# Kernel tuning notes

Hardware: AMD Instinct MI355X
Metric: run time of the kernel (lower is better)

The kernel has to match this reference:

```python
import jax, jax.numpy as jnp
import numpy as np

NUM_USERS = 100000
NUM_ITEMS = 50000
LATENT_DIM = 64
N_EDGES = 600000
BATCH = 4096
N_LAYERS = 4  # K=4, time_split=4, euler -> 4 unit propagation steps


def setup_inputs() -> dict:
    key = jax.random.key(0)
    k1, k2, k3, k4, k5, k6 = jax.random.split(key, 6)
    return {
        "users": jax.random.randint(k1, (BATCH,), 0, NUM_USERS),
        "items": jax.random.randint(k2, (BATCH,), 0, NUM_ITEMS),
        "edge_u": jax.random.randint(k3, (N_EDGES,), 0, NUM_USERS),
        "edge_i": jax.random.randint(k4, (N_EDGES,), 0, NUM_ITEMS),
        "user_emb": 0.1 * jax.random.normal(k5, (NUM_USERS, LATENT_DIM), dtype=jnp.float32),
        "item_emb": 0.1 * jax.random.normal(k6, (NUM_ITEMS, LATENT_DIM), dtype=jnp.float32),
    }


def reference(users, items, edge_u, edge_i, user_emb, item_emb):
    num_users = user_emb.shape[0]
    num_items = item_emb.shape[0]
    N = num_users + num_items

    # symmetric bipartite adjacency as directed edge list
    src = jnp.concatenate([edge_u, edge_i + num_users])
    dst = jnp.concatenate([edge_i + num_users, edge_u])

    # D^{-1/2} A D^{-1/2} edge weights (LightGCN normalization)
    deg = jax.ops.segment_sum(jnp.ones_like(src, dtype=jnp.float32), src, num_segments=N)
    inv_sqrt = jnp.where(deg > 0, jax.lax.rsqrt(jnp.maximum(deg, 1.0)), 0.0)
    w = inv_sqrt[src] * inv_sqrt[dst]  # [2E]

    def spmm(x):  # A_hat @ x via gather-scale-scatter
        return jax.ops.segment_sum(w[:, None] * x[src], dst, num_segments=N)

    x0 = jnp.concatenate([user_emb, item_emb], axis=0)  # [N, d]
    # ODE euler step x + A x, then residual subtraction -> stored emb = A^k x0
    embs = [x0]
    e = x0
    for _ in range(N_LAYERS):
        e = spmm(e)
        embs.append(e)
    light_out = jnp.mean(jnp.stack(embs, axis=1), axis=1)  # [N, d]

    all_users = light_out[:num_users]
    all_items = light_out[num_users:]
    users_emb = all_users[users]
    items_emb = all_items[items]
    gamma = jnp.sum(users_emb * items_emb, axis=1)  # [B]
    return gamma
```

## Files before the change

kernel.cpp:

```cpp
#include <hip/hip_runtime.h>

#define WAVE 64
#define BROWS 256
#define NBKT_MAX 1024
#define CMAX 4
#define SRCMASK 0x3FFFF
#define EPB 2048
#define ENTCAP 4096


__device__ __forceinline__ unsigned short f2bf(float f) {
    unsigned u = __float_as_uint(f);
    u += 0x7FFF + ((u >> 16) & 1);
    return (unsigned short)(u >> 16);
}
__device__ __forceinline__ float bf2f(unsigned short v) {
    return __uint_as_float((unsigned)v << 16);
}
__device__ __forceinline__ void addbf8(float* a, uint4 v) {
    a[0] += __uint_as_float(v.x << 16);
    a[1] += __uint_as_float(v.x & 0xFFFF0000u);
    a[2] += __uint_as_float(v.y << 16);
    a[3] += __uint_as_float(v.y & 0xFFFF0000u);
    a[4] += __uint_as_float(v.z << 16);
    a[5] += __uint_as_float(v.z & 0xFFFF0000u);
    a[6] += __uint_as_float(v.w << 16);
    a[7] += __uint_as_float(v.w & 0xFFFF0000u);
}

__global__ void k_hist(const int* __restrict__ eu, const int* __restrict__ ei,
                       int nE, int nU, int nBkt, int nJg, int* __restrict__ cntBB) {
    __shared__ int h4[4 * NBKT_MAX];
    for (int i = threadIdx.x; i < 4 * nBkt; i += 256) h4[i] = 0;
    __syncthreads();
    int* hw = h4 + (threadIdx.x >> 6) * nBkt;
    const int4* eu4 = (const int4*)eu;
    const int4* ei4 = (const int4*)ei;
    for (int pass = 0; pass < 2; pass++) {
        int i4 = blockIdx.x * 512 + pass * 256 + threadIdx.x;
        int e0 = i4 * 4;
        if (e0 + 3 < nE) {
            int4 u = eu4[i4];
            int4 v = ei4[i4];
            atomicAdd(&hw[u.x >> 8], 1); atomicAdd(&hw[(nU + v.x) >> 8], 1);
            atomicAdd(&hw[u.y >> 8], 1); atomicAdd(&hw[(nU + v.y) >> 8], 1);
            atomicAdd(&hw[u.z >> 8], 1); atomicAdd(&hw[(nU + v.z) >> 8], 1);
            atomicAdd(&hw[u.w >> 8], 1); atomicAdd(&hw[(nU + v.w) >> 8], 1);
        } else if (e0 < nE) {
            for (int e = e0; e < nE; e++) {
                atomicAdd(&hw[eu[e] >> 8], 1);
                atomicAdd(&hw[(nU + ei[e]) >> 8], 1);
            }
        }
    }
    __syncthreads();
    int j = (blockIdx.x & 7) * nJg + (blockIdx.x >> 3);
    int* dst = cntBB + (size_t)j * nBkt;
    for (int i = threadIdx.x; i < nBkt; i += 256)
        dst[i] = h4[i] + h4[nBkt + i] + h4[2 * nBkt + i] + h4[3 * nBkt + i];
}

__global__ void k_scanBkt(const int* __restrict__ cntBB, int* __restrict__ baseBB,
                          int* __restrict__ bktTot, int nBkt, int nJ) {
    __shared__ int s[256];
    int b = blockIdx.x, t = threadIdx.x;
    int C = (nJ + 255) / 256;
    int vals[CMAX];
    int sum = 0;
    for (int k = 0; k < CMAX; k++) {
        if (k >= C) break;
        int j = t * C + k;
        int v = (j < nJ) ? cntBB[(size_t)j * nBkt + b] : 0;
        vals[k] = v; sum += v;
    }
    s[t] = sum;
    __syncthreads();
    for (int o = 1; o < 256; o <<= 1) {
        int x = (t >= o) ? s[t - o] : 0;
        __syncthreads();
        s[t] += x;
        __syncthreads();
    }
    int run = s[t] - sum;
    for (int k = 0; k < CMAX; k++) {
        if (k >= C) break;
        int j = t * C + k;
        if (j < nJ) { baseBB[(size_t)b * nJ + j] = run; run += vals[k]; }
    }
    if (t == 0) bktTot[b] = s[255];
}

__global__ void k_scanTot(const int* __restrict__ bktTot, int* __restrict__ bktBase,
                          int* __restrict__ row_ptr, int nBkt, int N, int total) {
    __shared__ int s[1024];
    int t = threadIdx.x;
    int v = (t < nBkt) ? bktTot[t] : 0;
    s[t] = v;
    __syncthreads();
    for (int o = 1; o < 1024; o <<= 1) {
        int x = (t >= o) ? s[t - o] : 0;
        __syncthreads();
        s[t] += x;
        __syncthreads();
    }
    if (t < nBkt) bktBase[t] = s[t] - v;
    if (t == 0) { bktBase[nBkt] = total; row_ptr[N] = total; }
}

__global__ void k_bin(const int* __restrict__ eu, const int* __restrict__ ei,
                      int nE, int nU, int nBkt, int nJ, int nJg,
                      const int* __restrict__ baseBB, const int* __restrict__ bktBase,
                      int* __restrict__ bins) {
    __shared__ int cur[NBKT_MAX];
    int j = (blockIdx.x & 7) * nJg + (blockIdx.x >> 3);
    for (int i = threadIdx.x; i < nBkt; i += 256)
        cur[i] = bktBase[i] + baseBB[(size_t)i * nJ + j];
    __syncthreads();
    const int4* eu4 = (const int4*)eu;
    const int4* ei4 = (const int4*)ei;
    for (int pass = 0; pass < 2; pass++) {
        int i4 = blockIdx.x * 512 + pass * 256 + threadIdx.x;
        int e0 = i4 * 4;
        if (e0 + 3 < nE) {
            int4 uu = eu4[i4];
            int4 vv = ei4[i4];
            #pragma unroll
            for (int k = 0; k < 4; k++) {
                int u = (k == 0) ? uu.x : (k == 1) ? uu.y : (k == 2) ? uu.z : uu.w;
                int i2 = (k == 0) ? vv.x : (k == 1) ? vv.y : (k == 2) ? vv.z : vv.w;
                int v = nU + i2;
                int p1 = atomicAdd(&cur[u >> 8], 1);
                int p2 = atomicAdd(&cur[v >> 8], 1);
                bins[p1] = ((u & 255) << 18) | v;
                bins[p2] = ((v & 255) << 18) | u;
            }
        } else if (e0 < nE) {
            for (int e = e0; e < nE; e++) {
                int u = eu[e];
                int v = nU + ei[e];
                int p1 = atomicAdd(&cur[u >> 8], 1);
                int p2 = atomicAdd(&cur[v >> 8], 1);
                bins[p1] = ((u & 255) << 18) | v;
                bins[p2] = ((v & 255) << 18) | u;
            }
        }
    }
}

__global__ void k_csrz(const int* __restrict__ bins, const int* __restrict__ bktBase,
                       int N, int nU,
                       const float* __restrict__ ue, const float* __restrict__ ie,
                       int* __restrict__ row_ptr, int* __restrict__ col,
                       unsigned short* __restrict__ z0) {
    __shared__ int ent[ENTCAP];
    __shared__ int h4[4 * BROWS];
    __shared__ int sc[BROWS];
    __shared__ int cur4[4 * BROWS];
    __shared__ float sInv[BROWS];
    int b = blockIdx.x, t = threadIdx.x, w = t >> 6;
    int base = bktBase[b];
    int n = bktBase[b + 1] - base;
    h4[t] = 0; h4[256 + t] = 0; h4[512 + t] = 0; h4[768 + t] = 0;
    __syncthreads();
    int* hw = h4 + w * BROWS;
    for (int i = t; i < n; i += 256) {
        int p = bins[base + i];
        if (i < ENTCAP) ent[i] = p;
        atomicAdd(&hw[p >> 18], 1);
    }
    __syncthreads();
    int v = h4[t] + h4[256 + t] + h4[512 + t] + h4[768 + t];
    sc[t] = v;
    __syncthreads();
    for (int o = 1; o < 256; o <<= 1) {
        int x = (t >= o) ? sc[t - o] : 0;
        __syncthreads();
        sc[t] += x;
        __syncthreads();
    }
    int excl = sc[t] - v;
    int row = b * BROWS + t;
    if (row < N) row_ptr[row] = base + excl;
    sInv[t] = (v > 0) ? (1.0f / sqrtf((float)v)) : 0.0f;
    cur4[t]       = excl;
    cur4[256 + t] = excl + h4[t];
    cur4[512 + t] = excl + h4[t] + h4[256 + t];
    cur4[768 + t] = excl + h4[t] + h4[256 + t] + h4[512 + t];
    __syncthreads();
    int rf = t & 15, rg = t >> 4;
    for (int pass = 0; pass < 16; pass++) {
        int r = pass * 16 + rg;
        int rr = b * BROWS + r;
        if (rr < N) {
            const float4* src = (rr < nU)
                ? ((const float4*)ue) + (size_t)rr * 16
                : ((const float4*)ie) + (size_t)(rr - nU) * 16;
            float4 val = src[rf];
            float scl = sInv[r];
            ushort4 o;
            o.x = f2bf(val.x * scl);
            o.y = f2bf(val.y * scl);
            o.z = f2bf(val.z * scl);
            o.w = f2bf(val.w * scl);
            ((ushort4*)z0)[(size_t)rr * 16 + rf] = o;
        }
    }
    int* cw = cur4 + w * BROWS;
    for (int i = t; i < n; i += 256) {
        int p = (i < ENTCAP) ? ent[i] : bins[base + i];
        int pos = base + atomicAdd(&cw[p >> 18], 1);
        col[pos] = p & SRCMASK;
    }
}

__global__ void k_spmm(const int* __restrict__ row_ptr, const int* __restrict__ col,
                       const unsigned short* __restrict__ x,
                       unsigned short* __restrict__ y, int N, int nBlkMain,
                       const int* __restrict__ users, const int* __restrict__ items,
                       int B, int nU,
                       const float* __restrict__ ue, const float* __restrict__ ie,
                       float* __restrict__ acc, int mode) {
    int t = threadIdx.x;
    if ((int)blockIdx.x < nBlkMain) {
        int grp = t >> 3, f = t & 7;
        int row = blockIdx.x * 32 + grp;
        if (row >= N) return;
        const uint4* x8 = (const uint4*)x;
        int s = row_ptr[row], e = row_ptr[row + 1];
        float a0[8] = {0,0,0,0,0,0,0,0};
        float a1[8] = {0,0,0,0,0,0,0,0};
        float a2[8] = {0,0,0,0,0,0,0,0};
        float a3[8] = {0,0,0,0,0,0,0,0};
        for (int j = s; j < e; j += 8) {
            #pragma unroll
            for (int k = 0; k < 8; k++) {
                int jj = j + k;
                bool ok = jj < e;
                int c = col[ok ? jj : (e - 1)];
                uint4 v = x8[(size_t)c * 8 + f];
                if (!ok) { v.x = 0; v.y = 0; v.z = 0; v.w = 0; }
                if ((k & 3) == 0) addbf8(a0, v);
                else if ((k & 3) == 1) addbf8(a1, v);
                else if ((k & 3) == 2) addbf8(a2, v);
                else addbf8(a3, v);
            }
        }
        float rdeg = (e > s) ? (1.0f / (float)(e - s)) : 0.0f;
        uint4 o;
        float s0, s1;
        s0 = (a0[0]+a1[0]+a2[0]+a3[0]) * rdeg; s1 = (a0[1]+a1[1]+a2[1]+a3[1]) * rdeg;
        o.x = (unsigned)f2bf(s0) | ((unsigned)f2bf(s1) << 16);
        s0 = (a0[2]+a1[2]+a2[2]+a3[2]) * rdeg; s1 = (a0[3]+a1[3]+a2[3]+a3[3]) * rdeg;
        o.y = (unsigned)f2bf(s0) | ((unsigned)f2bf(s1) << 16);
        s0 = (a0[4]+a1[4]+a2[4]+a3[4]) * rdeg; s1 = (a0[5]+a1[5]+a2[5]+a3[5]) * rdeg;
        o.z = (unsigned)f2bf(s0) | ((unsigned)f2bf(s1) << 16);
        s0 = (a0[6]+a1[6]+a2[6]+a3[6]) * rdeg; s1 = (a0[7]+a1[7]+a2[7]+a3[7]) * rdeg;
        o.w = (unsigned)f2bf(s0) | ((unsigned)f2bf(s1) << 16);
        ((uint4*)y)[(size_t)row * 8 + f] = o;
    } else {
        int grp = t >> 4, f4 = t & 15;
        int b = (blockIdx.x - nBlkMain) * 16 + grp;
        if (b >= 2 * B) return;
        const ushort4* x4 = (const ushort4*)x;
        float4 c;
        if (mode == 0) {
            const float4* x0 = (b < B)
                ? ((const float4*)ue) + (size_t)users[b] * 16
                : ((const float4*)ie) + (size_t)items[b - B] * 16;
            c = x0[f4];
        } else {
            int row = (b < B) ? users[b] : (nU + items[b - B]);
            int deg = row_ptr[row + 1] - row_ptr[row];
            float f = sqrtf((float)deg);
            ushort4 v = x4[(size_t)row * 16 + f4];
            c = ((const float4*)acc)[(size_t)b * 16 + f4];
            c.x += f * bf2f(v.x); c.y += f * bf2f(v.y);
            c.z += f * bf2f(v.z); c.w += f * bf2f(v.w);
        }
        ((float4*)acc)[(size_t)b * 16 + f4] = c;
    }
}

__global__ void k_tail34(const int* __restrict__ row_ptr, const int* __restrict__ col,
                         const unsigned short* __restrict__ z3,
                         const int* __restrict__ users, const int* __restrict__ items,
                         int B, int nU, float* __restrict__ acc) {
    int t = threadIdx.x, grp = t >> 3, f = t & 7;
    int b = blockIdx.x * 32 + grp;
    if (b >= 2 * B) return;
    int row = (b < B) ? users[b] : (nU + items[b - B]);
    int s = row_ptr[row], e = row_ptr[row + 1];
    const uint4* x8 = (const uint4*)z3;
    float4 cA = ((const float4*)acc)[(size_t)b * 16 + 2 * f];
    float4 cB = ((const float4*)acc)[(size_t)b * 16 + 2 * f + 1];
    if (e > s) {
        float fq = sqrtf((float)(e - s));
        float a0[8] = {0,0,0,0,0,0,0,0};
        float a1[8] = {0,0,0,0,0,0,0,0};
        int j = s;
        for (; j + 1 < e; j += 2) {
            uint4 v0 = x8[(size_t)col[j] * 8 + f];
            uint4 v1 = x8[(size_t)col[j + 1] * 8 + f];
            addbf8(a0, v0); addbf8(a1, v1);
        }
        if (j < e) {
            uint4 v0 = x8[(size_t)col[j] * 8 + f];
            addbf8(a0, v0);
        }
        uint4 vs = x8[(size_t)row * 8 + f];
        float self[8] = {0,0,0,0,0,0,0,0};
        addbf8(self, vs);
        float scale = fq / (float)(e - s);
        cA.x += fq * self[0] + scale * (a0[0] + a1[0]);
        cA.y += fq * self[1] + scale * (a0[1] + a1[1]);
        cA.z += fq * self[2] + scale * (a0[2] + a1[2]);
        cA.w += fq * self[3] + scale * (a0[3] + a1[3]);
        cB.x += fq * self[4] + scale * (a0[4] + a1[4]);
        cB.y += fq * self[5] + scale * (a0[5] + a1[5]);
        cB.z += fq * self[6] + scale * (a0[6] + a1[6]);
        cB.w += fq * self[7] + scale * (a0[7] + a1[7]);
    }
    ((float4*)acc)[(size_t)b * 16 + 2 * f]     = cA;
    ((float4*)acc)[(size_t)b * 16 + 2 * f + 1] = cB;
}

__global__ void k_dot(const float* __restrict__ acc, int B, float* __restrict__ out) {
    int b = blockIdx.x * (blockDim.x >> 6) + (threadIdx.x >> 6);
    int lane = threadIdx.x & 63;
    if (b >= B) return;
    float p = acc[(size_t)b * 64 + lane] * acc[(size_t)(b + B) * 64 + lane];
    #pragma unroll
    for (int o = 32; o > 0; o >>= 1) p += __shfl_down(p, o, WAVE);
    if (lane == 0) out[b] = p * (1.0f / 25.0f);
}

extern "C" void kernel_launch(void* const* d_in, const int* in_sizes, int n_in,
                              void* d_out, int out_size, void* d_ws, size_t ws_size,
                              hipStream_t stream) {
    const int*   users = (const int*)d_in[0];
    const int*   items = (const int*)d_in[1];
    const int*   eu    = (const int*)d_in[2];
    const int*   ei    = (const int*)d_in[3];
    const float* ue    = (const float*)d_in[4];
    const float* ie    = (const float*)d_in[5];
    float* out = (float*)d_out;

    const int D  = 64;
    const int B  = in_sizes[0];
    const int nE = in_sizes[2];
    const int nU = in_sizes[4] / D;
    const int nI = in_sizes[5] / D;
    const int N  = nU + nI;
    const int nBkt = (N + BROWS - 1) / BROWS;
    const int total = 2 * nE;

    const int nBlkB = (nE + EPB - 1) / EPB;
    const int nJg   = (nBlkB + 7) / 8;
    const int nJ    = 8 * nJg;

    char* p = (char*)d_ws;
    auto alloc = [&](size_t bytes) -> void* {
        void* r = (void*)p;
        p += (bytes + 255) & ~(size_t)255;
        return r;
    };
    int*   cntBB   = (int*)  alloc((size_t)nJ * nBkt * 4);
    int*   baseBB  = (int*)  alloc((size_t)nBkt * nJ * 4);
    int*   bktTot  = (int*)  alloc((size_t)nBkt * 4);
    int*   bktBase = (int*)  alloc((size_t)(nBkt + 1) * 4);
    int*   bins    = (int*)  alloc((size_t)total * 4);
    int*   col     = (int*)  alloc((size_t)total * 4);
    int*   row_ptr = (int*)  alloc((size_t)(N + 1) * 4);
    unsigned short* za = (unsigned short*)alloc((size_t)N * D * 2);
    unsigned short* zb = (unsigned short*)alloc((size_t)N * D * 2);
    float* acc     = (float*)alloc((size_t)2 * B * D * 4);

    k_hist<<<nJ, 256, 0, stream>>>(eu, ei, nE, nU, nBkt, nJg, cntBB);
    k_scanBkt<<<nBkt, 256, 0, stream>>>(cntBB, baseBB, bktTot, nBkt, nJ);
    k_scanTot<<<1, 1024, 0, stream>>>(bktTot, bktBase, row_ptr, nBkt, N, total);
    k_bin<<<nJ, 256, 0, stream>>>(eu, ei, nE, nU, nBkt, nJ, nJg, baseBB, bktBase, bins);
    k_csrz<<<nBkt, BROWS, 0, stream>>>(bins, bktBase, N, nU, ue, ie, row_ptr, col, za);

    const int nBlkMain = (N + 31) / 32;
    const int nBlkTail = (2 * B + 15) / 16;
    unsigned short* zin = za;
    unsigned short* zout = zb;
    for (int l = 0; l < 3; l++) {
        k_spmm<<<nBlkMain + nBlkTail, 256, 0, stream>>>(
            row_ptr, col, zin, zout, N, nBlkMain,
            users, items, B, nU, ue, ie, acc, (l == 0) ? 0 : 1);
        unsigned short* t = zin; zin = zout; zout = t;
    }

    const int nBlkT34 = (2 * B + 31) / 32;
    k_tail34<<<nBlkT34, 256, 0, stream>>>(row_ptr, col, zin, users, items, B, nU, acc);
    k_dot<<<(B + 3) / 4, 256, 0, stream>>>(acc, B, out);
}
```

Measured before the change: 215.5 us.

## Stage edge binning in shared memory for coalesced bucket writes

The binning kernel now builds a per-block local histogram of bucket counts and scans it. Each block then scatters its 4096 entries into shared memory sorted by bucket and writes them to global memory in contiguous runs, where before every entry was scattered randomly. The aim is to make the global writes of the bins array far more coalesced. The cost is extra shared-memory atomics, a block-wide scan, more synchronisation and heavier shared-memory use, which may lower occupancy. Partial tail blocks keep the old direct-scatter path.

```diff
diff --git a/kernel.cpp b/kernel.cpp
--- a/kernel.cpp
+++ b/kernel.cpp
@@ -111,17 +111,41 @@
                       int nE, int nU, int nBkt, int nJ, int nJg,
                       const int* __restrict__ baseBB, const int* __restrict__ bktBase,
                       int* __restrict__ bins) {
-    __shared__ int cur[NBKT_MAX];
+    __shared__ int ent[2 * EPB];
+    __shared__ unsigned short ebkt[2 * EPB];
+    __shared__ int h2[2 * NBKT_MAX];
+    __shared__ int lcur[NBKT_MAX];
+    __shared__ int dlt[NBKT_MAX];
+    __shared__ int sp[256];
+    int t = threadIdx.x;
     int j = (blockIdx.x & 7) * nJg + (blockIdx.x >> 3);
-    for (int i = threadIdx.x; i < nBkt; i += 256)
-        cur[i] = bktBase[i] + baseBB[(size_t)i * nJ + j];
-    __syncthreads();
-    const int4* eu4 = (const int4*)eu;
-    const int4* ei4 = (const int4*)ei;
-    for (int pass = 0; pass < 2; pass++) {
-        int i4 = blockIdx.x * 512 + pass * 256 + threadIdx.x;
-        int e0 = i4 * 4;
-        if (e0 + 3 < nE) {
+    const bool fullBlk = ((size_t)(blockIdx.x + 1) * EPB <= (size_t)nE);
+
+    if (!fullBlk) {
+        for (int i = t; i < nBkt; i += 256)
+            lcur[i] = bktBase[i] + baseBB[(size_t)i * nJ + j];
+        __syncthreads();
+        for (int e = blockIdx.x * EPB + t; e < nE; e += 256) {
+            int u = eu[e];
+            int v = nU + ei[e];
+            int p1 = atomicAdd(&lcur[u >> 8], 1);
+            int p2 = atomicAdd(&lcur[v >> 8], 1);
+            bins[p1] = ((u & 255) << 18) | v;
+            bins[p2] = ((v & 255) << 18) | u;
+        }
+        return;
+    }
+
+    for (int i = t; i < nBkt; i += 256) { h2[i] = 0; h2[NBKT_MAX + i] = 0; }
+    __syncthreads();
+    int myb[16], mye[16];
+    int* hs = h2 + (t >> 7) * NBKT_MAX;
+    {
+        const int4* eu4 = (const int4*)eu;
+        const int4* ei4 = (const int4*)ei;
+        #pragma unroll
+        for (int pass = 0; pass < 2; pass++) {
+            int i4 = blockIdx.x * 512 + pass * 256 + t;
             int4 uu = eu4[i4];
             int4 vv = ei4[i4];
             #pragma unroll
@@ -129,22 +153,54 @@
                 int u = (k == 0) ? uu.x : (k == 1) ? uu.y : (k == 2) ? uu.z : uu.w;
                 int i2 = (k == 0) ? vv.x : (k == 1) ? vv.y : (k == 2) ? vv.z : vv.w;
                 int v = nU + i2;
-                int p1 = atomicAdd(&cur[u >> 8], 1);
-                int p2 = atomicAdd(&cur[v >> 8], 1);
-                bins[p1] = ((u & 255) << 18) | v;
-                bins[p2] = ((v & 255) << 18) | u;
+                int idx = pass * 8 + k * 2;
+                myb[idx]     = u >> 8; mye[idx]     = ((u & 255) << 18) | v;
+                myb[idx + 1] = v >> 8; mye[idx + 1] = ((v & 255) << 18) | u;
             }
-        } else if (e0 < nE) {
-            for (int e = e0; e < nE; e++) {
-                int u = eu[e];
-                int v = nU + ei[e];
-                int p1 = atomicAdd(&cur[u >> 8], 1);
-                int p2 = atomicAdd(&cur[v >> 8], 1);
-                bins[p1] = ((u & 255) << 18) | v;
-                bins[p2] = ((v & 255) << 18) | u;
-            }
-        }
-    }
+        }
+    }
+    #pragma unroll
+    for (int k = 0; k < 16; k++) atomicAdd(&hs[myb[k]], 1);
+    __syncthreads();
+    int C = (nBkt + 255) / 256;
+    int vals[4];
+    int sum = 0;
+    for (int k = 0; k < 4; k++) {
+        if (k >= C) break;
+        int b = t * C + k;
+        int v = (b < nBkt) ? (h2[b] + h2[NBKT_MAX + b]) : 0;
+        vals[k] = v; sum += v;
+    }
+    sp[t] = sum;
+    __syncthreads();
+    for (int o = 1; o < 256; o <<= 1) {
+        int x = (t >= o) ? sp[t - o] : 0;
+        __syncthreads();
+        sp[t] += x;
+        __syncthreads();
+    }
+    int run = sp[t] - sum;
+    for (int k = 0; k < 4; k++) {
+        if (k >= C) break;
+        int b = t * C + k;
+        if (b < nBkt) {
+            lcur[b] = run;
+            int g = bktBase[b] + baseBB[(size_t)b * nJ + j];
+            dlt[b] = g - run;
+            run += vals[k];
+        }
+    }
+    __syncthreads();
+    int n4 = sp[255];
+    #pragma unroll
+    for (int k = 0; k < 16; k++) {
+        int p = atomicAdd(&lcur[myb[k]], 1);
+        ent[p] = mye[k];
+        ebkt[p] = (unsigned short)myb[k];
+    }
+    __syncthreads();
+    for (int i = t; i < n4; i += 256)
+        bins[dlt[ebkt[i]] + i] = ent[i];
 }
 
 __global__ void k_csrz(const int* __restrict__ bins, const int* __restrict__ bktBase,
```

Result: faster. 210.8 us, median of 2 (-2.1%).
